# Performance work log

Measured on AMD Instinct MI355X. Metric: run time of the kernel, lower is better.

## Reference

```python
import jax, jax.numpy as jnp
import numpy as np

NUM_HEADS = 8


def setup_inputs() -> dict:
    key = jax.random.key(0)
    ks = jax.random.split(key, 16)
    B, C = 4, 512
    size = (8, 16, 16)
    def w(k):
        return jax.random.normal(k, (C, C), dtype=jnp.float32) * 0.02
    z = lambda: jnp.zeros((C,), jnp.float32)
    return {
        'x1': jax.random.normal(ks[0], (B, C) + size, dtype=jnp.float32),
        'x2': jax.random.normal(ks[1], (B, C) + size, dtype=jnp.float32),
        'Wq': w(ks[2]), 'bq': z(),
        'Wk': w(ks[3]), 'bk': z(),
        'Wv1': w(ks[4]), 'bv1': z(),
        'Wv2': w(ks[5]), 'bv2': z(),
        'Wo1': w(ks[6]), 'bo1': z(),
        'Wo2': w(ks[7]), 'bo2': z(),
    }


def reference(x1, x2, Wq, bq, Wk, bk, Wv1, bv1, Wv2, bv2, Wo1, bo1, Wo2, bo2):
    B, C = x1.shape[:2]
    size = x1.shape[2:]              # spatial dims, e.g. (8,16,16)
    N = int(np.prod(size))           # tokens
    dh = C // NUM_HEADS
    # flatten spatial -> (B, N, C)
    h1 = x1.reshape(B, C, N).transpose(0, 2, 1)
    h2 = x2.reshape(B, C, N).transpose(0, 2, 1)

    def heads(x):                    # (B,N,C) -> (B,H,N,dh)
        return x.reshape(B, N, NUM_HEADS, dh).transpose(0, 2, 1, 3)

    q = heads(h1 @ Wq + bq)
    k = heads(h2 @ Wk + bk)
    v1 = heads(h1 @ Wv1 + bv1)
    v2 = heads(h2 @ Wv2 + bv2)

    scores = jnp.einsum('bhqd,bhkd->bhqk', q, k) / jnp.sqrt(jnp.float32(dh))
    p1 = jax.nn.softmax(scores, axis=-2)                      # normalize over queries
    p2 = jnp.swapaxes(jax.nn.softmax(scores, axis=-1), -1, -2)  # (B,H,Nk,Nq)

    ctx1 = jnp.einsum('bhqk,bhkd->bhqd', p1, v1)
    ctx2 = jnp.einsum('bhkq,bhqd->bhkd', p2, v2)

    def merge(ctx):                  # (B,H,N,dh) -> (B,N,C)
        return ctx.transpose(0, 2, 1, 3).reshape(B, N, C)

    o1 = (merge(ctx1) @ Wo1 + bo1).transpose(0, 2, 1).reshape((B, C) + size) + x1
    o2 = (merge(ctx2) @ Wo2 + bo2).transpose(0, 2, 1).reshape((B, C) + size) + x2
    return (o1, o2)
```

## Files before the change

kernel.cpp:

```cpp
#include <hip/hip_runtime.h>

typedef __attribute__((ext_vector_type(8))) __bf16 bf16x8;
typedef __attribute__((ext_vector_type(4))) float f32x4;
typedef __attribute__((ext_vector_type(16))) float f32x16;
typedef unsigned int u32;

#define MFMA32(a, b, c) __builtin_amdgcn_mfma_f32_32x32x16_bf16((a), (b), (c), 0, 0, 0)
#define EXP2(x) __builtin_amdgcn_exp2f(x)
#define SETPRIO(n) __builtin_amdgcn_s_setprio(n)

static constexpr int Bsz = 4, C = 512, N = 2048, H = 8, DH = 64;
static constexpr int BN = Bsz * N;
static constexpr size_t BCN = (size_t)Bsz * C * N;
static constexpr float SM_C = 0.18033688011112042f;

__device__ __forceinline__ void gload16(const void* g, void* lds) {
  __builtin_amdgcn_global_load_lds(
      (const __attribute__((address_space(1))) u32*)g,
      (__attribute__((address_space(3))) u32*)lds, 16, 0, 0);
}

__device__ __forceinline__ u32 cvt_pk_bf16(float lo, float hi) {
  u32 r;
  asm("v_cvt_pk_bf16_f32 %0, %1, %2" : "=v"(r) : "v"(lo), "v"(hi));
  return r;
}

__device__ __forceinline__ void permswap32(u32& a, u32& b) {
  asm volatile("v_permlane32_swap_b32 %0, %1" : "+v"(a), "+v"(b));
}

static constexpr size_t SZ_BF = (size_t)BN * C * sizeof(__bf16);
static constexpr size_t SZ_W  = (size_t)C * C * sizeof(__bf16);
static constexpr size_t SZ_ST = (size_t)Bsz * H * N * sizeof(float);
static constexpr size_t OFF_HT1  = 0;
static constexpr size_t OFF_HT2  = OFF_HT1 + SZ_BF;
static constexpr size_t OFF_Q    = OFF_HT2 + SZ_BF;
static constexpr size_t OFF_K    = OFF_Q + SZ_BF;
static constexpr size_t OFF_VT1  = OFF_K + SZ_BF;
static constexpr size_t OFF_VT2  = OFF_VT1 + SZ_BF;
static constexpr size_t OFF_CTX1 = OFF_VT2 + SZ_BF;
static constexpr size_t OFF_CTX2 = OFF_CTX1 + SZ_BF;
static constexpr size_t OFF_WQT  = OFF_CTX2 + SZ_BF;
static constexpr size_t OFF_WKT  = OFF_WQT + SZ_W;
static constexpr size_t OFF_WV1T = OFF_WKT + SZ_W;
static constexpr size_t OFF_WV2T = OFF_WV1T + SZ_W;
static constexpr size_t OFF_WO1T = OFF_WV2T + SZ_W;
static constexpr size_t OFF_WO2T = OFF_WO1T + SZ_W;
static constexpr size_t OFF_QS   = OFF_WO2T + SZ_W;
static constexpr size_t OFF_KS   = OFF_QS + SZ_ST;

__global__ __launch_bounds__(256) void k_tc2(const float* __restrict__ x1,
                                             const float* __restrict__ x2,
                                             __bf16* __restrict__ h1,
                                             __bf16* __restrict__ h2) {
  __shared__ __bf16 tile[64][66];
  int z = blockIdx.z;
  size_t boff = (size_t)(z & 3) * C * N;
  const float* src = (z < 4 ? x1 : x2) + boff;
  __bf16* dst = (z < 4 ? h1 : h2) + boff;
  int r0 = blockIdx.y * 64, c0 = blockIdx.x * 64;
  int t = threadIdx.x;
  int cl = t & 63, rr = t >> 6;
#pragma unroll
  for (int i = 0; i < 16; ++i) {
    int r = rr * 16 + i;
    tile[r][cl] = (__bf16)src[(size_t)(r0 + r) * N + c0 + cl];
  }
  __syncthreads();
#pragma unroll
  for (int i = 0; i < 16; ++i) {
    int c = rr * 16 + i;
    dst[(size_t)(c0 + c) * C + r0 + cl] = tile[cl][c];
  }
}

struct WT6 {
  const float* src[6];
  __bf16* dst[6];
};
__global__ __launch_bounds__(256) void k_tcw(WT6 p) {
  __shared__ __bf16 tile[64][66];
  int z = blockIdx.z;
  const float* src = p.src[z];
  __bf16* dst = p.dst[z];
  int r0 = blockIdx.y * 64, c0 = blockIdx.x * 64;
  int t = threadIdx.x;
  int cl = t & 63, rr = t >> 6;
#pragma unroll
  for (int i = 0; i < 16; ++i) {
    int r = rr * 16 + i;
    tile[r][cl] = (__bf16)src[(size_t)(r0 + r) * C + c0 + cl];
  }
  __syncthreads();
#pragma unroll
  for (int i = 0; i < 16; ++i) {
    int c = rr * 16 + i;
    dst[(size_t)(c0 + c) * C + r0 + cl] = tile[cl][c];
  }
}

struct GArgs {
  const __bf16* A; const __bf16* Bt; const float* bias; const float* rs;
  __bf16* outb; float* outf; const float* resid; float scale;
};

template <int MODE>
__global__ __launch_bounds__(256, 2) void k_gemm(GArgs g0, GArgs g1) {
  __shared__ __bf16 As[2 * 128 * 64];
  __shared__ __bf16 Bs[2 * 128 * 64];
  int lin = blockIdx.x;
  int swz = (lin & 7) * 64 + (lin >> 3);
  int dir = swz >> 8;
  int inner = swz & 255;
  const __bf16* Ap = dir ? g1.A : g0.A;
  const __bf16* Bp = dir ? g1.Bt : g0.Bt;
  const float* bias = dir ? g1.bias : g0.bias;
  const float* rs = dir ? g1.rs : g0.rs;
  __bf16* outb = dir ? g1.outb : g0.outb;
  float* outf = dir ? g1.outf : g0.outf;
  const float* resid = dir ? g1.resid : g0.resid;
  float scale = dir ? g1.scale : g0.scale;
  int m0 = (inner & 63) * 128, n0 = (inner >> 6) * 128;
  int t = threadIdx.x, lane = t & 63, w = t >> 6;
  int wm = w >> 1, wn = w & 1;
  int l31 = lane & 31, hi = lane >> 5;
  int srow = t >> 3;
  int sc8 = ((t & 7) ^ (srow & 7)) * 8;
  int swA = (l31 & 7) << 4;
  int aoff0 = (wm * 64 + l31) * 128;
  int aoff1 = (wm * 64 + 32 + l31) * 128;
  int boff0 = (wn * 64 + l31) * 128;
  int boff1 = (wn * 64 + 32 + l31) * 128;
  f32x16 acc[2][2] = {};

#define GSTAGE(p, k0)                                                        \
  {                                                                          \
    _Pragma("unroll") for (int gI = 0; gI < 4; ++gI) {                       \
      int row_ = gI * 32 + srow;                                             \
      gload16(&Ap[(size_t)(m0 + row_) * C + (k0) + sc8],                     \
              (char*)As + (p) * 16384 + gI * 4096 + w * 1024);               \
      gload16(&Bp[(size_t)(n0 + row_) * C + (k0) + sc8],                     \
              (char*)Bs + (p) * 16384 + gI * 4096 + w * 1024);               \
    }                                                                        \
  }

  GSTAGE(0, 0)
  __syncthreads();
  for (int ks = 0; ks < 8; ++ks) {
    int p = ks & 1;
    if (ks < 7) GSTAGE(p ^ 1, (ks + 1) * 64)
    const char* ab = (const char*)As + p * 16384;
    const char* bb = (const char*)Bs + p * 16384;
    int ko0 = (hi * 16) ^ swA;
    bf16x8 a0c = *(const bf16x8*)(ab + aoff0 + ko0);
    bf16x8 a1c = *(const bf16x8*)(ab + aoff1 + ko0);
    bf16x8 b0c = *(const bf16x8*)(bb + boff0 + ko0);
    bf16x8 b1c = *(const bf16x8*)(bb + boff1 + ko0);
#pragma unroll
    for (int kk = 0; kk < 4; ++kk) {
      bf16x8 a0n, a1n, b0n, b1n;
      if (kk < 3) {
        int ko = ((kk + 1) * 32 + hi * 16) ^ swA;
        a0n = *(const bf16x8*)(ab + aoff0 + ko);
        a1n = *(const bf16x8*)(ab + aoff1 + ko);
        b0n = *(const bf16x8*)(bb + boff0 + ko);
        b1n = *(const bf16x8*)(bb + boff1 + ko);
      }
      acc[0][0] = MFMA32(a0c, b0c, acc[0][0]);
      acc[0][1] = MFMA32(a0c, b1c, acc[0][1]);
      acc[1][0] = MFMA32(a1c, b0c, acc[1][0]);
      acc[1][1] = MFMA32(a1c, b1c, acc[1][1]);
      if (kk < 3) { a0c = a0n; a1c = a1n; b0c = b0n; b1c = b1n; }
    }
    __syncthreads();
  }
#pragma unroll
  for (int mi = 0; mi < 2; ++mi)
#pragma unroll
    for (int ni = 0; ni < 2; ++ni) {
      int gn = n0 + wn * 64 + ni * 32 + l31;
      float bv = bias[gn];
#pragma unroll
      for (int g2 = 0; g2 < 4; ++g2) {
        int gm = m0 + wm * 64 + mi * 32 + 8 * g2 + 4 * hi;
        int b = gm >> 11, n = gm & 2047;
        if (MODE == 0) {
          int h = gn >> 6, d = gn & 63;
          size_t base = (size_t)(b * 8 + h) * 2048 + n;
#pragma unroll
          for (int j = 0; j < 4; ++j)
            outb[(base + j) * 64 + d] = (__bf16)((acc[mi][ni][4 * g2 + j] + bv) * scale);
        } else if (MODE == 1) {
          int h = gn >> 6, d = gn & 63;
          size_t tok = (size_t)(b * 8 + h) * 2048 + n;
          float4 sv = *reinterpret_cast<const float4*>(&rs[tok]);
          size_t addr = ((size_t)(b * 8 + h) * 64 + d) * 2048 + n;
          union { __bf16 h4[4]; uint2 u; } pk;
          pk.h4[0] = (__bf16)((acc[mi][ni][4 * g2 + 0] + bv) * __builtin_amdgcn_rcpf(sv.x));
          pk.h4[1] = (__bf16)((acc[mi][ni][4 * g2 + 1] + bv) * __builtin_amdgcn_rcpf(sv.y));
          pk.h4[2] = (__bf16)((acc[mi][ni][4 * g2 + 2] + bv) * __builtin_amdgcn_rcpf(sv.z));
          pk.h4[3] = (__bf16)((acc[mi][ni][4 * g2 + 3] + bv) * __builtin_amdgcn_rcpf(sv.w));
          *reinterpret_cast<uint2*>(&outb[addr]) = pk.u;
        } else {
          size_t addr = ((size_t)b * C + gn) * 2048 + n;
          float4 xv = *reinterpret_cast<const float4*>(&resid[addr]);
          float4 ov;
          ov.x = acc[mi][ni][4 * g2 + 0] + bv + xv.x;
          ov.y = acc[mi][ni][4 * g2 + 1] + bv + xv.y;
          ov.z = acc[mi][ni][4 * g2 + 2] + bv + xv.z;
          ov.w = acc[mi][ni][4 * g2 + 3] + bv + xv.w;
          *reinterpret_cast<float4*>(&outf[addr]) = ov;
        }
      }
    }
}

struct SArgs { const __bf16* X; const __bf16* Y; float* ors; };

__global__ __launch_bounds__(256, 6) void k_stats(SArgs sa0, SArgs sa1) {
  __shared__ __bf16 Ys[2 * 64 * 64];
  int lin = blockIdx.x;
  int swz = (lin & 7) * 128 + (lin >> 3);
  int dir = swz >> 9;
  int inner = swz & 511;
  const __bf16* X = dir ? sa1.X : sa0.X;
  const __bf16* Y = dir ? sa1.Y : sa0.Y;
  float* ors = dir ? sa1.ors : sa0.ors;
  int bh = inner >> 4, xblk = inner & 15;
  int t = threadIdx.x, lane = t & 63, w = t >> 6;
  int l31 = lane & 31, hi = lane >> 5;
  const __bf16* Xb = X + (size_t)bh * N * DH;
  const __bf16* Yb = Y + (size_t)bh * N * DH;
  int qg = xblk * 128 + w * 32 + l31;
  bf16x8 xq[4];
#pragma unroll
  for (int kk = 0; kk < 4; ++kk)
    xq[kk] = *(const bf16x8*)&Xb[(size_t)qg * DH + kk * 16 + hi * 8];
  int srow = t >> 3;
  int sc8 = ((t & 7) ^ (srow & 7)) * 8;
  int ybase = l31 * 128;
  int sw = (l31 & 7) << 4;
#define SSTAGE(p, kc2)                                                       \
  {                                                                          \
    char* yb_ = (char*)Ys + (p) * 8192 + w * 1024;                           \
    gload16(&Yb[(size_t)((kc2) + srow) * DH + sc8], yb_);                    \
    gload16(&Yb[(size_t)((kc2) + 32 + srow) * DH + sc8], yb_ + 4096);        \
  }
  float sa_ = 0.f, sb_ = 0.f;
  SSTAGE(0, 0)
  __syncthreads();
  for (int it = 0; it < 32; ++it) {
    int p = it & 1;
    if (it < 31) SSTAGE(p ^ 1, (it + 1) * 64)
    const char* yb = (const char*)Ys + p * 8192;
#pragma unroll
    for (int cblk = 0; cblk < 2; ++cblk) {
      f32x16 s0 = {};
      SETPRIO(1);
#pragma unroll
      for (int kk = 0; kk < 4; ++kk) {
        bf16x8 yf = *(const bf16x8*)(yb + cblk * 4096 + ybase +
                                     ((kk * 32 + hi * 16) ^ sw));
        s0 = MFMA32(yf, xq[kk], s0);
      }
      SETPRIO(0);
#pragma unroll
      for (int e = 0; e < 8; ++e) {
        sa_ += EXP2(s0[e]);
        sb_ += EXP2(s0[e + 8]);
      }
    }
    __syncthreads();
  }
  float sum0 = sa_ + sb_;
  sum0 += __shfl_xor(sum0, 32, 64);
  if (hi == 0) ors[(size_t)bh * N + qg] = sum0;
}

struct CArgs { const __bf16* X; const __bf16* Y; const __bf16* Vt; __bf16* out; };

__global__ __launch_bounds__(256, 4) void k_ctx(CArgs c0, CArgs c1) {
  __shared__ __bf16 Ys[2 * 64 * 64];
  __shared__ __bf16 Vs[2 * 64 * 64];
  int lin = blockIdx.x;
  int swz = (lin & 7) * 128 + (lin >> 3);
  int dir = swz >> 9;
  int inner = swz & 511;
  const __bf16* X = dir ? c1.X : c0.X;
  const __bf16* Y = dir ? c1.Y : c0.Y;
  const __bf16* Vt = dir ? c1.Vt : c0.Vt;
  __bf16* out = dir ? c1.out : c0.out;
  int bh = inner >> 4, xblk = inner & 15;
  int b = bh >> 3, h = bh & 7;
  int t = threadIdx.x, lane = t & 63, w = t >> 6;
  int l31 = lane & 31, hi = lane >> 5;
  const __bf16* Xb = X + (size_t)bh * N * DH;
  const __bf16* Yb = Y + (size_t)bh * N * DH;
  const __bf16* Vb = Vt + (size_t)bh * DH * N;
  int qg = xblk * 128 + w * 32 + l31;
  bf16x8 xq[4];
#pragma unroll
  for (int kk = 0; kk < 4; ++kk)
    xq[kk] = *(const bf16x8*)&Xb[(size_t)qg * DH + kk * 16 + hi * 8];
  int srow = t >> 3;
  int sc8 = ((t & 7) ^ (srow & 7)) * 8;
  int ybase = l31 * 128;
  int sw = (l31 & 7) << 4;
#define CSTAGE(p, kc2)                                                        \
  {                                                                           \
    char* yb_ = (char*)Ys + (p) * 8192 + w * 1024;                            \
    char* vb_ = (char*)Vs + (p) * 8192 + w * 1024;                            \
    gload16(&Yb[(size_t)((kc2) + srow) * DH + sc8], yb_);                     \
    gload16(&Yb[(size_t)((kc2) + 32 + srow) * DH + sc8], yb_ + 4096);         \
    gload16(&Vb[(size_t)srow * N + (kc2) + sc8], vb_);                        \
    gload16(&Vb[(size_t)(32 + srow) * N + (kc2) + sc8], vb_ + 4096);          \
  }
  f32x16 oacc[2] = {};
  CSTAGE(0, 0)
  __syncthreads();
  for (int it = 0; it < 32; ++it) {
    int p = it & 1;
    if (it < 31) CSTAGE(p ^ 1, (it + 1) * 64)
    const char* yb = (const char*)Ys + p * 8192;
    const char* vb = (const char*)Vs + p * 8192;
#pragma unroll
    for (int cblk = 0; cblk < 2; ++cblk) {
      f32x16 s0 = {};
      SETPRIO(1);
#pragma unroll
      for (int kk = 0; kk < 4; ++kk) {
        bf16x8 yf = *(const bf16x8*)(yb + cblk * 4096 + ybase +
                                     ((kk * 32 + hi * 16) ^ sw));
        s0 = MFMA32(yf, xq[kk], s0);
      }
      SETPRIO(0);
      u32 wl0[4], wh0[4];
#pragma unroll
      for (int g = 0; g < 4; ++g) {
        wl0[g] = cvt_pk_bf16(EXP2(s0[4 * g + 0]), EXP2(s0[4 * g + 1]));
        wh0[g] = cvt_pk_bf16(EXP2(s0[4 * g + 2]), EXP2(s0[4 * g + 3]));
      }
#pragma unroll
      for (int sh = 0; sh < 2; ++sh) {
        int ct = cblk * 2 + sh;
        u32 p00 = wl0[2 * sh], p01 = wl0[2 * sh + 1];
        u32 p02 = wh0[2 * sh], p03 = wh0[2 * sh + 1];
        permswap32(p00, p01);
        permswap32(p02, p03);
        union { u32 wd[4]; bf16x8 v; } pf0;
        pf0.wd[0] = p00; pf0.wd[1] = p02; pf0.wd[2] = p01; pf0.wd[3] = p03;
        SETPRIO(1);
#pragma unroll
        for (int dblk = 0; dblk < 2; ++dblk) {
          bf16x8 vf = *(const bf16x8*)(vb + (dblk * 32 + l31) * 128 +
                                       ((ct * 32 + hi * 16) ^ sw));
          oacc[dblk] = MFMA32(vf, pf0.v, oacc[dblk]);
        }
        SETPRIO(0);
      }
    }
    __syncthreads();
  }
#pragma unroll
  for (int dblk = 0; dblk < 2; ++dblk)
#pragma unroll
    for (int g = 0; g < 4; ++g) {
      union { __bf16 h4[4]; uint2 u; } pk;
#pragma unroll
      for (int m = 0; m < 4; ++m) pk.h4[m] = (__bf16)oacc[dblk][4 * g + m];
      int d = dblk * 32 + 8 * g + 4 * hi;
      size_t addr = ((size_t)b * N + qg) * C + h * 64 + d;
      *reinterpret_cast<uint2*>(&out[addr]) = pk.u;
    }
}

extern "C" void kernel_launch(void* const* d_in, const int* in_sizes, int n_in,
                              void* d_out, int out_size, void* d_ws, size_t ws_size,
                              hipStream_t stream) {
  (void)in_sizes; (void)n_in; (void)out_size; (void)ws_size;
  const float* x1  = (const float*)d_in[0];
  const float* x2  = (const float*)d_in[1];
  const float* Wq  = (const float*)d_in[2];
  const float* bq  = (const float*)d_in[3];
  const float* Wk  = (const float*)d_in[4];
  const float* bk  = (const float*)d_in[5];
  const float* Wv1 = (const float*)d_in[6];
  const float* bv1 = (const float*)d_in[7];
  const float* Wv2 = (const float*)d_in[8];
  const float* bv2 = (const float*)d_in[9];
  const float* Wo1 = (const float*)d_in[10];
  const float* bo1 = (const float*)d_in[11];
  const float* Wo2 = (const float*)d_in[12];
  const float* bo2 = (const float*)d_in[13];

  char* ws = (char*)d_ws;
  __bf16* ht1  = (__bf16*)(ws + OFF_HT1);
  __bf16* ht2  = (__bf16*)(ws + OFF_HT2);
  __bf16* qb   = (__bf16*)(ws + OFF_Q);
  __bf16* kb   = (__bf16*)(ws + OFF_K);
  __bf16* vt1  = (__bf16*)(ws + OFF_VT1);
  __bf16* vt2  = (__bf16*)(ws + OFF_VT2);
  __bf16* ctx1 = (__bf16*)(ws + OFF_CTX1);
  __bf16* ctx2 = (__bf16*)(ws + OFF_CTX2);
  __bf16* wqt  = (__bf16*)(ws + OFF_WQT);
  __bf16* wkt  = (__bf16*)(ws + OFF_WKT);
  __bf16* wv1t = (__bf16*)(ws + OFF_WV1T);
  __bf16* wv2t = (__bf16*)(ws + OFF_WV2T);
  __bf16* wo1t = (__bf16*)(ws + OFF_WO1T);
  __bf16* wo2t = (__bf16*)(ws + OFF_WO2T);
  float* qs = (float*)(ws + OFF_QS);
  float* ks = (float*)(ws + OFF_KS);
  float* outf = (float*)d_out;

  dim3 blk(256);
  k_tc2<<<dim3(32, 8, 8), blk, 0, stream>>>(x1, x2, ht1, ht2);
  WT6 wt;
  wt.src[0] = Wq;  wt.dst[0] = wqt;
  wt.src[1] = Wk;  wt.dst[1] = wkt;
  wt.src[2] = Wv1; wt.dst[2] = wv1t;
  wt.src[3] = Wv2; wt.dst[3] = wv2t;
  wt.src[4] = Wo1; wt.dst[4] = wo1t;
  wt.src[5] = Wo2; wt.dst[5] = wo2t;
  k_tcw<<<dim3(8, 8, 6), blk, 0, stream>>>(wt);

  GArgs gq0{ht1, wqt, bq, nullptr, qb, nullptr, nullptr, SM_C};
  GArgs gq1{ht2, wkt, bk, nullptr, kb, nullptr, nullptr, 1.0f};
  k_gemm<0><<<512, blk, 0, stream>>>(gq0, gq1);

  SArgs st0{qb, kb, qs};
  SArgs st1{kb, qb, ks};
  k_stats<<<1024, blk, 0, stream>>>(st0, st1);

  GArgs gv0{ht1, wv1t, bv1, ks, vt1, nullptr, nullptr, 0.f};
  GArgs gv1{ht2, wv2t, bv2, qs, vt2, nullptr, nullptr, 0.f};
  k_gemm<1><<<512, blk, 0, stream>>>(gv0, gv1);

  CArgs cc0{qb, kb, vt1, ctx1};
  CArgs cc1{kb, qb, vt2, ctx2};
  k_ctx<<<1024, blk, 0, stream>>>(cc0, cc1);

  GArgs go0{ctx1, wo1t, bo1, nullptr, nullptr, outf, x1, 0.f};
  GArgs go1{ctx2, wo2t, bo2, nullptr, nullptr, outf + BCN, x2, 0.f};
  k_gemm<2><<<512, blk, 0, stream>>>(go0, go1);
}
```

Before: 192.7 us.

## Fuse Q/K/V projections into one GEMM launch and apply softmax normalization in ctx

The four input projections (Q, K, V1, V2) now run in a single 1024-block launch. To allow that, the V projection no longer depends on the softmax column sums. The stats kernel stores reciprocal sums, and the ctx kernel stages them into LDS per key tile and multiplies them into the exponentials before the PV MFMA. The merged GEMM drops LDS double buffering for four blocks per CU, and the output GEMM loses its register prefetch of fragments. The aim is to remove a launch and a serial dependency, at the cost of extra multiplies and LDS reads in the ctx inner loop and less load/compute overlap in the GEMMs.

```diff
diff --git a/kernel.cpp b/kernel.cpp
--- a/kernel.cpp
+++ b/kernel.cpp
@@ -18,6 +18,11 @@
   __builtin_amdgcn_global_load_lds(
       (const __attribute__((address_space(1))) u32*)g,
       (__attribute__((address_space(3))) u32*)lds, 16, 0, 0);
+}
+__device__ __forceinline__ void gload4(const void* g, void* lds) {
+  __builtin_amdgcn_global_load_lds(
+      (const __attribute__((address_space(1))) u32*)g,
+      (__attribute__((address_space(3))) u32*)lds, 4, 0, 0);
 }
 
 __device__ __forceinline__ u32 cvt_pk_bf16(float lo, float hi) {
@@ -100,27 +105,20 @@
   }
 }
 
-struct GArgs {
-  const __bf16* A; const __bf16* Bt; const float* bias; const float* rs;
-  __bf16* outb; float* outf; const float* resid; float scale;
+struct GArgs4 {
+  const __bf16* A; const __bf16* Bt; const float* bias;
+  __bf16* outb; float scale; int mode;
 };
 
-template <int MODE>
-__global__ __launch_bounds__(256, 2) void k_gemm(GArgs g0, GArgs g1) {
-  __shared__ __bf16 As[2 * 128 * 64];
-  __shared__ __bf16 Bs[2 * 128 * 64];
+__global__ __launch_bounds__(256, 4) void k_gemm4(GArgs4 g0, GArgs4 g1,
+                                                  GArgs4 g2, GArgs4 g3) {
+  __shared__ __bf16 As[128 * 64];
+  __shared__ __bf16 Bs[128 * 64];
   int lin = blockIdx.x;
-  int swz = (lin & 7) * 64 + (lin >> 3);
-  int dir = swz >> 8;
+  int swz = (lin & 7) * 128 + (lin >> 3);
+  int sub = swz >> 8;
   int inner = swz & 255;
-  const __bf16* Ap = dir ? g1.A : g0.A;
-  const __bf16* Bp = dir ? g1.Bt : g0.Bt;
-  const float* bias = dir ? g1.bias : g0.bias;
-  const float* rs = dir ? g1.rs : g0.rs;
-  __bf16* outb = dir ? g1.outb : g0.outb;
-  float* outf = dir ? g1.outf : g0.outf;
-  const float* resid = dir ? g1.resid : g0.resid;
-  float scale = dir ? g1.scale : g0.scale;
+  GArgs4 ga = (sub == 0) ? g0 : (sub == 1) ? g1 : (sub == 2) ? g2 : g3;
   int m0 = (inner & 63) * 128, n0 = (inner >> 6) * 128;
   int t = threadIdx.x, lane = t & 63, w = t >> 6;
   int wm = w >> 1, wn = w & 1;
@@ -134,7 +132,93 @@
   int boff1 = (wn * 64 + 32 + l31) * 128;
   f32x16 acc[2][2] = {};
 
-#define GSTAGE(p, k0)                                                        \
+  for (int ks = 0; ks < 8; ++ks) {
+    int k0 = ks * 64;
+#pragma unroll
+    for (int gI = 0; gI < 4; ++gI) {
+      int row_ = gI * 32 + srow;
+      gload16(&ga.A[(size_t)(m0 + row_) * C + k0 + sc8],
+              (char*)As + gI * 4096 + w * 1024);
+      gload16(&ga.Bt[(size_t)(n0 + row_) * C + k0 + sc8],
+              (char*)Bs + gI * 4096 + w * 1024);
+    }
+    __syncthreads();
+    const char* ab = (const char*)As;
+    const char* bb = (const char*)Bs;
+#pragma unroll
+    for (int kk = 0; kk < 4; ++kk) {
+      int ko = (kk * 32 + hi * 16) ^ swA;
+      bf16x8 a0 = *(const bf16x8*)(ab + aoff0 + ko);
+      bf16x8 a1 = *(const bf16x8*)(ab + aoff1 + ko);
+      bf16x8 b0 = *(const bf16x8*)(bb + boff0 + ko);
+      bf16x8 b1 = *(const bf16x8*)(bb + boff1 + ko);
+      acc[0][0] = MFMA32(a0, b0, acc[0][0]);
+      acc[0][1] = MFMA32(a0, b1, acc[0][1]);
+      acc[1][0] = MFMA32(a1, b0, acc[1][0]);
+      acc[1][1] = MFMA32(a1, b1, acc[1][1]);
+    }
+    __syncthreads();
+  }
+#pragma unroll
+  for (int mi = 0; mi < 2; ++mi)
+#pragma unroll
+    for (int ni = 0; ni < 2; ++ni) {
+      int gn = n0 + wn * 64 + ni * 32 + l31;
+      float bv = ga.bias[gn];
+      int h = gn >> 6, d = gn & 63;
+#pragma unroll
+      for (int g2 = 0; g2 < 4; ++g2) {
+        int gm = m0 + wm * 64 + mi * 32 + 8 * g2 + 4 * hi;
+        int b = gm >> 11, n = gm & 2047;
+        if (ga.mode == 0) {
+          size_t base = (size_t)(b * 8 + h) * 2048 + n;
+#pragma unroll
+          for (int j = 0; j < 4; ++j)
+            ga.outb[(base + j) * 64 + d] =
+                (__bf16)((acc[mi][ni][4 * g2 + j] + bv) * ga.scale);
+        } else {
+          size_t addr = ((size_t)(b * 8 + h) * 64 + d) * 2048 + n;
+          union { __bf16 h4[4]; uint2 u; } pk;
+#pragma unroll
+          for (int j = 0; j < 4; ++j)
+            pk.h4[j] = (__bf16)(acc[mi][ni][4 * g2 + j] + bv);
+          *reinterpret_cast<uint2*>(&ga.outb[addr]) = pk.u;
+        }
+      }
+    }
+}
+
+struct GArgsO {
+  const __bf16* A; const __bf16* Bt; const float* bias;
+  float* outf; const float* resid;
+};
+
+__global__ __launch_bounds__(256, 2) void k_gemmO(GArgsO g0, GArgsO g1) {
+  __shared__ __bf16 As[2 * 128 * 64];
+  __shared__ __bf16 Bs[2 * 128 * 64];
+  int lin = blockIdx.x;
+  int swz = (lin & 7) * 64 + (lin >> 3);
+  int dir = swz >> 8;
+  int inner = swz & 255;
+  const __bf16* Ap = dir ? g1.A : g0.A;
+  const __bf16* Bp = dir ? g1.Bt : g0.Bt;
+  const float* bias = dir ? g1.bias : g0.bias;
+  float* outf = dir ? g1.outf : g0.outf;
+  const float* resid = dir ? g1.resid : g0.resid;
+  int m0 = (inner & 63) * 128, n0 = (inner >> 6) * 128;
+  int t = threadIdx.x, lane = t & 63, w = t >> 6;
+  int wm = w >> 1, wn = w & 1;
+  int l31 = lane & 31, hi = lane >> 5;
+  int srow = t >> 3;
+  int sc8 = ((t & 7) ^ (srow & 7)) * 8;
+  int swA = (l31 & 7) << 4;
+  int aoff0 = (wm * 64 + l31) * 128;
+  int aoff1 = (wm * 64 + 32 + l31) * 128;
+  int boff0 = (wn * 64 + l31) * 128;
+  int boff1 = (wn * 64 + 32 + l31) * 128;
+  f32x16 acc[2][2] = {};
+
+#define OSTAGE(p, k0)                                                        \
   {                                                                          \
     _Pragma("unroll") for (int gI = 0; gI < 4; ++gI) {                       \
       int row_ = gI * 32 + srow;                                             \
@@ -145,33 +229,24 @@
     }                                                                        \
   }
 
-  GSTAGE(0, 0)
+  OSTAGE(0, 0)
   __syncthreads();
   for (int ks = 0; ks < 8; ++ks) {
     int p = ks & 1;
-    if (ks < 7) GSTAGE(p ^ 1, (ks + 1) * 64)
+    if (ks < 7) OSTAGE(p ^ 1, (ks + 1) * 64)
     const char* ab = (const char*)As + p * 16384;
     const char* bb = (const char*)Bs + p * 16384;
-    int ko0 = (hi * 16) ^ swA;
-    bf16x8 a0c = *(const bf16x8*)(ab + aoff0 + ko0);
-    bf16x8 a1c = *(const bf16x8*)(ab + aoff1 + ko0);
-    bf16x8 b0c = *(const bf16x8*)(bb + boff0 + ko0);
-    bf16x8 b1c = *(const bf16x8*)(bb + boff1 + ko0);
 #pragma unroll
     for (int kk = 0; kk < 4; ++kk) {
-      bf16x8 a0n, a1n, b0n, b1n;
-      if (kk < 3) {
-        int ko = ((kk + 1) * 32 + hi * 16) ^ swA;
-        a0n = *(const bf16x8*)(ab + aoff0 + ko);
-        a1n = *(const bf16x8*)(ab + aoff1 + ko);
-        b0n = *(const bf16x8*)(bb + boff0 + ko);
-        b1n = *(const bf16x8*)(bb + boff1 + ko);
-      }
-      acc[0][0] = MFMA32(a0c, b0c, acc[0][0]);
-      acc[0][1] = MFMA32(a0c, b1c, acc[0][1]);
-      acc[1][0] = MFMA32(a1c, b0c, acc[1][0]);
-      acc[1][1] = MFMA32(a1c, b1c, acc[1][1]);
-      if (kk < 3) { a0c = a0n; a1c = a1n; b0c = b0n; b1c = b1n; }
+      int ko = (kk * 32 + hi * 16) ^ swA;
+      bf16x8 a0 = *(const bf16x8*)(ab + aoff0 + ko);
+      bf16x8 a1 = *(const bf16x8*)(ab + aoff1 + ko);
+      bf16x8 b0 = *(const bf16x8*)(bb + boff0 + ko);
+      bf16x8 b1 = *(const bf16x8*)(bb + boff1 + ko);
+      acc[0][0] = MFMA32(a0, b0, acc[0][0]);
+      acc[0][1] = MFMA32(a0, b1, acc[0][1]);
+      acc[1][0] = MFMA32(a1, b0, acc[1][0]);
+      acc[1][1] = MFMA32(a1, b1, acc[1][1]);
     }
     __syncthreads();
   }
@@ -185,33 +260,14 @@
       for (int g2 = 0; g2 < 4; ++g2) {
         int gm = m0 + wm * 64 + mi * 32 + 8 * g2 + 4 * hi;
         int b = gm >> 11, n = gm & 2047;
-        if (MODE == 0) {
-          int h = gn >> 6, d = gn & 63;
-          size_t base = (size_t)(b * 8 + h) * 2048 + n;
-#pragma unroll
-          for (int j = 0; j < 4; ++j)
-            outb[(base + j) * 64 + d] = (__bf16)((acc[mi][ni][4 * g2 + j] + bv) * scale);
-        } else if (MODE == 1) {
-          int h = gn >> 6, d = gn & 63;
-          size_t tok = (size_t)(b * 8 + h) * 2048 + n;
-          float4 sv = *reinterpret_cast<const float4*>(&rs[tok]);
-          size_t addr = ((size_t)(b * 8 + h) * 64 + d) * 2048 + n;
-          union { __bf16 h4[4]; uint2 u; } pk;
-          pk.h4[0] = (__bf16)((acc[mi][ni][4 * g2 + 0] + bv) * __builtin_amdgcn_rcpf(sv.x));
-          pk.h4[1] = (__bf16)((acc[mi][ni][4 * g2 + 1] + bv) * __builtin_amdgcn_rcpf(sv.y));
-          pk.h4[2] = (__bf16)((acc[mi][ni][4 * g2 + 2] + bv) * __builtin_amdgcn_rcpf(sv.z));
-          pk.h4[3] = (__bf16)((acc[mi][ni][4 * g2 + 3] + bv) * __builtin_amdgcn_rcpf(sv.w));
-          *reinterpret_cast<uint2*>(&outb[addr]) = pk.u;
-        } else {
-          size_t addr = ((size_t)b * C + gn) * 2048 + n;
-          float4 xv = *reinterpret_cast<const float4*>(&resid[addr]);
-          float4 ov;
-          ov.x = acc[mi][ni][4 * g2 + 0] + bv + xv.x;
-          ov.y = acc[mi][ni][4 * g2 + 1] + bv + xv.y;
-          ov.z = acc[mi][ni][4 * g2 + 2] + bv + xv.z;
-          ov.w = acc[mi][ni][4 * g2 + 3] + bv + xv.w;
-          *reinterpret_cast<float4*>(&outf[addr]) = ov;
-        }
+        size_t addr = ((size_t)b * C + gn) * 2048 + n;
+        float4 xv = *reinterpret_cast<const float4*>(&resid[addr]);
+        float4 ov;
+        ov.x = acc[mi][ni][4 * g2 + 0] + bv + xv.x;
+        ov.y = acc[mi][ni][4 * g2 + 1] + bv + xv.y;
+        ov.z = acc[mi][ni][4 * g2 + 2] + bv + xv.z;
+        ov.w = acc[mi][ni][4 * g2 + 3] + bv + xv.w;
+        *reinterpret_cast<float4*>(&outf[addr]) = ov;
       }
     }
 }
@@ -275,14 +331,18 @@
   }
   float sum0 = sa_ + sb_;
   sum0 += __shfl_xor(sum0, 32, 64);
-  if (hi == 0) ors[(size_t)bh * N + qg] = sum0;
-}
-
-struct CArgs { const __bf16* X; const __bf16* Y; const __bf16* Vt; __bf16* out; };
+  if (hi == 0) ors[(size_t)bh * N + qg] = __builtin_amdgcn_rcpf(sum0);
+}
+
+struct CArgs {
+  const __bf16* X; const __bf16* Y; const __bf16* Vt;
+  const float* rs; __bf16* out;
+};
 
 __global__ __launch_bounds__(256, 4) void k_ctx(CArgs c0, CArgs c1) {
   __shared__ __bf16 Ys[2 * 64 * 64];
   __shared__ __bf16 Vs[2 * 64 * 64];
+  __shared__ float RsL[2][64];
   int lin = blockIdx.x;
   int swz = (lin & 7) * 128 + (lin >> 3);
   int dir = swz >> 9;
@@ -290,6 +350,7 @@
   const __bf16* X = dir ? c1.X : c0.X;
   const __bf16* Y = dir ? c1.Y : c0.Y;
   const __bf16* Vt = dir ? c1.Vt : c0.Vt;
+  const float* rs = dir ? c1.rs : c0.rs;
   __bf16* out = dir ? c1.out : c0.out;
   int bh = inner >> 4, xblk = inner & 15;
   int b = bh >> 3, h = bh & 7;
@@ -298,6 +359,7 @@
   const __bf16* Xb = X + (size_t)bh * N * DH;
   const __bf16* Yb = Y + (size_t)bh * N * DH;
   const __bf16* Vb = Vt + (size_t)bh * DH * N;
+  const float* rb = rs + (size_t)bh * N;
   int qg = xblk * 128 + w * 32 + l31;
   bf16x8 xq[4];
 #pragma unroll
@@ -315,6 +377,7 @@
     gload16(&Yb[(size_t)((kc2) + 32 + srow) * DH + sc8], yb_ + 4096);         \
     gload16(&Vb[(size_t)srow * N + (kc2) + sc8], vb_);                        \
     gload16(&Vb[(size_t)(32 + srow) * N + (kc2) + sc8], vb_ + 4096);          \
+    if (w == 0) gload4(&rb[(kc2) + lane], &RsL[p][0]);                        \
   }
   f32x16 oacc[2] = {};
   CSTAGE(0, 0)
@@ -338,8 +401,11 @@
       u32 wl0[4], wh0[4];
 #pragma unroll
       for (int g = 0; g < 4; ++g) {
-        wl0[g] = cvt_pk_bf16(EXP2(s0[4 * g + 0]), EXP2(s0[4 * g + 1]));
-        wh0[g] = cvt_pk_bf16(EXP2(s0[4 * g + 2]), EXP2(s0[4 * g + 3]));
+        f32x4 rv = *(const f32x4*)&RsL[p][cblk * 32 + 8 * g + 4 * hi];
+        wl0[g] = cvt_pk_bf16(EXP2(s0[4 * g + 0]) * rv[0],
+                             EXP2(s0[4 * g + 1]) * rv[1]);
+        wh0[g] = cvt_pk_bf16(EXP2(s0[4 * g + 2]) * rv[2],
+                             EXP2(s0[4 * g + 3]) * rv[3]);
       }
 #pragma unroll
       for (int sh = 0; sh < 2; ++sh) {
@@ -424,23 +490,21 @@
   wt.src[5] = Wo2; wt.dst[5] = wo2t;
   k_tcw<<<dim3(8, 8, 6), blk, 0, stream>>>(wt);
 
-  GArgs gq0{ht1, wqt, bq, nullptr, qb, nullptr, nullptr, SM_C};
-  GArgs gq1{ht2, wkt, bk, nullptr, kb, nullptr, nullptr, 1.0f};
-  k_gemm<0><<<512, blk, 0, stream>>>(gq0, gq1);
+  GArgs4 pq{ht1, wqt, bq, qb, SM_C, 0};
+  GArgs4 pk{ht2, wkt, bk, kb, 1.0f, 0};
+  GArgs4 pv1{ht1, wv1t, bv1, vt1, 0.f, 1};
+  GArgs4 pv2{ht2, wv2t, bv2, vt2, 0.f, 1};
+  k_gemm4<<<1024, blk, 0, stream>>>(pq, pk, pv1, pv2);
 
   SArgs st0{qb, kb, qs};
   SArgs st1{kb, qb, ks};
   k_stats<<<1024, blk, 0, stream>>>(st0, st1);
 
-  GArgs gv0{ht1, wv1t, bv1, ks, vt1, nullptr, nullptr, 0.f};
-  GArgs gv1{ht2, wv2t, bv2, qs, vt2, nullptr, nullptr, 0.f};
-  k_gemm<1><<<512, blk, 0, stream>>>(gv0, gv1);
-
-  CArgs cc0{qb, kb, vt1, ctx1};
-  CArgs cc1{kb, qb, vt2, ctx2};
+  CArgs cc0{qb, kb, vt1, ks, ctx1};
+  CArgs cc1{kb, qb, vt2, qs, ctx2};
   k_ctx<<<1024, blk, 0, stream>>>(cc0, cc1);
 
-  GArgs go0{ctx1, wo1t, bo1, nullptr, nullptr, outf, x1, 0.f};
-  GArgs go1{ctx2, wo2t, bo2, nullptr, nullptr, outf + BCN, x2, 0.f};
-  k_gemm<2><<<512, blk, 0, stream>>>(go0, go1);
-}
+  GArgsO go0{ctx1, wo1t, bo1, outf, x1};
+  GArgsO go1{ctx2, wo2t, bo2, outf + BCN, x2};
+  k_gemmO<<<512, blk, 0, stream>>>(go0, go1);
+}
```

Result: no change. 196.2 us (+1.8%).
